# Optimization experiments

Measured on AMD Instinct MI355X. Metric: run time of the kernel, lower is better.

## Reference

```python
import jax, jax.numpy as jnp
import numpy as np


def setup_inputs() -> dict:
    key = jax.random.key(0)
    k1, k2, k3, k4 = jax.random.split(key, 4)
    B, N, F = 16, 2048, 512
    return {
        "source": jax.random.normal(k1, (B, N, 3), dtype=jnp.float32),
        "target": jax.random.normal(k2, (B, N, 3), dtype=jnp.float32),
        "fsource": jax.random.normal(k3, (B, F, N), dtype=jnp.float32),
        "ftarget": jax.random.normal(k4, (B, F, N), dtype=jnp.float32),
    }


def reference(source, target, fsource, ftarget):
    # source/target: (B, N, 3) -> (B, 3, N)
    src = jnp.swapaxes(source, 1, 2)
    tgt = jnp.swapaxes(target, 1, 2)

    # soft correspondence: logits[b, i, j] = <ftarget[b,:,i], fsource[b,:,j]>
    logits = jnp.einsum('bfi,bfj->bij', ftarget, fsource)  # (B, Nt, Ns)
    weight = jax.nn.softmax(logits, axis=1)  # softmax over target points (dim=1)

    # predicted target for each source point: (B, 3, Ns)
    pred_tgt = jnp.einsum('bci,bij->bcj', tgt, weight)

    src_mean = jnp.mean(src, axis=2, keepdims=True)        # (B, 3, 1)
    tgt_mean = jnp.mean(pred_tgt, axis=2, keepdims=True)   # (B, 3, 1)
    src_res = src - src_mean
    tgt_res = pred_tgt - tgt_mean

    # 3x3 cross-covariance per batch item
    S = jnp.einsum('bcn,bdn->bcd', src_res, tgt_res)  # (B, 3, 3)

    # torch.svd: S = U diag(Sig) V^T ; jnp.linalg.svd: S = U diag(Sig) Vh
    U, Sig, Vh = jnp.linalg.svd(S, full_matrices=False)
    V = jnp.swapaxes(Vh, 1, 2)
    UT = jnp.swapaxes(U, 1, 2)

    d = jnp.linalg.det(jnp.matmul(V, UT))  # (B,)
    B = S.shape[0]
    M = jnp.tile(jnp.eye(3, dtype=S.dtype)[None], (B, 1, 1))
    M = M.at[:, 2, 2].set(d)

    Rot = jnp.matmul(jnp.matmul(V, M), UT)                     # (B, 3, 3)
    tr = (tgt_mean - jnp.matmul(Rot, src_mean))[..., 0]        # (B, 3)
    return (Rot, tr)
```

## Files before the change

### kernel.cpp

```cpp
#include <hip/hip_runtime.h>
#include <math.h>
#include <stdint.h>

#define NB   16
#define NPT  2048
#define NF   512
#define BI   128
#define BJ   128
#define KB   32
#define NTHR 512
#define NJT  (NPT / BJ)
#define NIT  (NPT / BI)
#define NKC  (NF / KB)
#define NIQ  4

#define CGB1     1024
#define KCSLAB1  (128 * CGB1)
#define TPB1     ((size_t)NB * NKC * KCSLAB1)

#define CGS    1056
#define PLANE  8448
#define PLANE_H 4224
#define BPLANE 16896
#define BUF2   50688

typedef _Float16 h4 __attribute__((ext_vector_type(4)));
typedef _Float16 h8 __attribute__((ext_vector_type(8)));
typedef float    f32x4 __attribute__((ext_vector_type(4)));

#define TRR(dst, a) asm volatile("ds_read_b64_tr_b16 %0, %1" : "=v"(dst) : "v"(a))

#define MF(A, B, C) __builtin_amdgcn_mfma_f32_16x16x32_f16(A, B, C, 0, 0, 0)

__device__ __forceinline__ void gld16(const void* g, void* l) {
    __builtin_amdgcn_global_load_lds(
        (const __attribute__((address_space(1))) unsigned int*)g,
        (__attribute__((address_space(3))) unsigned int*)l, 16, 0, 0);
}

__device__ __forceinline__ h8 cat(h4 a, h4 b) {
    return __builtin_shufflevector(a, b, 0, 1, 2, 3, 4, 5, 6, 7);
}

__device__ __forceinline__ void cvt8(const float4 a, const float4 b, h8& hi, h8& lo) {
    hi[0] = (_Float16)a.x; hi[1] = (_Float16)a.y;
    hi[2] = (_Float16)a.z; hi[3] = (_Float16)a.w;
    hi[4] = (_Float16)b.x; hi[5] = (_Float16)b.y;
    hi[6] = (_Float16)b.z; hi[7] = (_Float16)b.w;
    lo[0] = (_Float16)(a.x - (float)hi[0]);
    lo[1] = (_Float16)(a.y - (float)hi[1]);
    lo[2] = (_Float16)(a.z - (float)hi[2]);
    lo[3] = (_Float16)(a.w - (float)hi[3]);
    lo[4] = (_Float16)(b.x - (float)hi[4]);
    lo[5] = (_Float16)(b.y - (float)hi[5]);
    lo[6] = (_Float16)(b.z - (float)hi[6]);
    lo[7] = (_Float16)(b.w - (float)hi[7]);
}

__device__ __forceinline__ h8 cvt8h(const float4 a, const float4 b) {
    h8 hi;
    hi[0] = (_Float16)a.x; hi[1] = (_Float16)a.y;
    hi[2] = (_Float16)a.z; hi[3] = (_Float16)a.w;
    hi[4] = (_Float16)b.x; hi[5] = (_Float16)b.y;
    hi[6] = (_Float16)b.z; hi[7] = (_Float16)b.w;
    return hi;
}

__device__ __forceinline__ int hoffB(int f, int n8) {
    return (n8 >> 1) * CGS + (f >> 4) * 512 + ((f >> 2) & 3) * 128
         + (f & 3) * 32 + (n8 & 1) * 16;
}

__global__ __launch_bounds__(256)
void prepass_kernel(const float* __restrict__ fsource,
                    const float* __restrict__ ftarget,
                    _Float16* __restrict__ tiled)
{
    const int b  = blockIdx.x;
    const int kc = blockIdx.y;
    const int z  = blockIdx.z;
    const int tensor = z >> 3;
    const int cgrp   = z & 7;
    const float* src = (tensor == 0 ? ftarget : fsource)
                     + (size_t)b * NF * NPT + (size_t)kc * KB * NPT + cgrp * 256;
    char* dst = (char*)tiled + (size_t)tensor * TPB1
              + ((size_t)(b * NKC + kc) * 128 + cgrp * 16) * CGB1;

    __shared__ _Float16 sm[8448];
    const int t   = threadIdx.x;
    const int kk8 = t >> 5;
    const int c8  = (t & 31) * 8;
    const int cg  = c8 >> 4;
    const int cl  = c8 & 15;

    #pragma unroll
    for (int rep = 0; rep < 4; ++rep) {
        const int k = rep * 8 + kk8;
        const float4 v0 = *(const float4*)(src + (size_t)k * NPT + c8);
        const float4 v1 = *(const float4*)(src + (size_t)k * NPT + c8 + 4);
        const h8 hi = cvt8h(v0, v1);
        const int kh = k >> 4, kr = k & 15, kg = kr >> 2, j = kr & 3;
        *(h8*)((char*)sm + cg * 1056 + kh * 512 + kg * 128 + j * 32 + cl * 2) = hi;
    }
    __syncthreads();
    #pragma unroll
    for (int q = 0; q < 4; ++q) {
        const int off = q * 4096 + t * 16;
        const int ocg = off >> 10, rem = off & 1023;
        *(float4*)(dst + off) = *(const float4*)((char*)sm + ocg * 1056 + rem);
    }
}

__global__ __launch_bounds__(256, 2)
void attn_state_tiled(const float* __restrict__ target,
                      const _Float16* __restrict__ tiled,
                      float* __restrict__ stw)
{
    const int b    = blockIdx.x;
    const int jt   = blockIdx.y;
    const int iq   = blockIdx.z;
    const int j0   = jt * BJ;
    const int tid  = threadIdx.x;
    const int lane = tid & 63;
    const int wave = tid >> 6;
    const int wi   = wave >> 1;
    const int wj   = wave & 1;
    const int lg   = lane >> 4;
    const int lr   = lane & 15;

    __shared__ __align__(16) char TIL[2][32768];
    __shared__ float  tgtsAll[3][512];
    __shared__ float  redM[2][BJ];
    __shared__ float4 redS[2][BJ];

    const uint32_t tilesBase = (uint32_t)(uintptr_t)&TIL[0][0];
    const uint32_t trLane    = (uint32_t)(lane * 8);

    const char* Atile = (const char*)tiled;
    const char* Btile = (const char*)tiled + TPB1;

    {
        const float* tg = target + ((size_t)b * NPT + iq * 512) * 3;
        #pragma unroll
        for (int k = 0; k < 6; ++k) {
            const int p = tid + k * 256;
            tgtsAll[p % 3][p / 3] = tg[p];
        }
    }
    __syncthreads();

    float Mrun[4], Zrun[4], Yrun[4][3];
    #pragma unroll
    for (int n = 0; n < 4; ++n) {
        Mrun[n] = -3.0e38f; Zrun[n] = 0.0f;
        Yrun[n][0] = 0.0f; Yrun[n][1] = 0.0f; Yrun[n][2] = 0.0f;
    }

#define STAGE2(kc2v, dstbuf) { \
    const size_t slab0 = (size_t)(b * NKC + 2 * (kc2v)) * KCSLAB1; \
    const size_t slab1 = slab0 + KCSLAB1; \
    const size_t aoff  = (size_t)(i0 >> 4) * CGB1 + lane * 16; \
    const size_t boff  = (size_t)(j0 >> 4) * CGB1 + lane * 16; \
    char* lb = &TIL[dstbuf][0]; \
    gld16(Atile + slab0 + aoff + wave * 1024,       lb + wave * 1024); \
    gld16(Atile + slab0 + aoff + (wave + 4) * 1024, lb + (wave + 4) * 1024); \
    gld16(Atile + slab1 + aoff + wave * 1024,       lb + 8192 + wave * 1024); \
    gld16(Atile + slab1 + aoff + (wave + 4) * 1024, lb + 8192 + (wave + 4) * 1024); \
    gld16(Btile + slab0 + boff + wave * 1024,       lb + 16384 + wave * 1024); \
    gld16(Btile + slab0 + boff + (wave + 4) * 1024, lb + 16384 + (wave + 4) * 1024); \
    gld16(Btile + slab1 + boff + wave * 1024,       lb + 24576 + wave * 1024); \
    gld16(Btile + slab1 + boff + (wave + 4) * 1024, lb + 24576 + (wave + 4) * 1024); }

#define RD_A1(m) TRR(ta[m][0], aB + (m) * CGB1); \
                 TRR(ta[m][1], aB + (m) * CGB1 + 512);
#define RD_B1(n) TRR(tb[n][0], bB + (n) * CGB1); \
                 TRR(tb[n][1], bB + (n) * CGB1 + 512);
#define WAITK(N) asm volatile("s_waitcnt lgkmcnt(" #N ")" ::: "memory"); \
                 __builtin_amdgcn_sched_barrier(0);
#define MROW1(M) \
    { const h8 Ah = cat(ta[M][0], ta[M][1]); \
      acc[M][0] = MF(Ah, Bh[0], acc[M][0]); \
      acc[M][1] = MF(Ah, Bh[1], acc[M][1]); \
      acc[M][2] = MF(Ah, Bh[2], acc[M][2]); \
      acc[M][3] = MF(Ah, Bh[3], acc[M][3]); }

#define KHALF(hofs) { \
    const uint32_t aB = bufB + (hofs) + (uint32_t)(wi * 4) * CGB1 + trLane; \
    const uint32_t bB = bufB + 16384u + (hofs) + (uint32_t)(wj * 4) * CGB1 + trLane; \
    h4 ta[4][2], tb[4][2]; \
    h8 Bh[4]; \
    RD_A1(0) RD_B1(0) RD_B1(1) RD_B1(2) RD_B1(3) \
    RD_A1(1) RD_A1(2) RD_A1(3) \
    WAITK(6) \
    Bh[0] = cat(tb[0][0], tb[0][1]); \
    Bh[1] = cat(tb[1][0], tb[1][1]); \
    Bh[2] = cat(tb[2][0], tb[2][1]); \
    Bh[3] = cat(tb[3][0], tb[3][1]); \
    MROW1(0) \
    WAITK(4) MROW1(1) \
    WAITK(2) MROW1(2) \
    WAITK(0) MROW1(3) }

    for (int it = 0; it < 4; ++it) {
        const int i0 = iq * 512 + it * BI;

        STAGE2(0, 0)
        asm volatile("s_waitcnt vmcnt(0)" ::: "memory");
        __builtin_amdgcn_sched_barrier(0);
        __syncthreads();

        f32x4 acc[4][4];
        #pragma unroll
        for (int m = 0; m < 4; ++m)
            #pragma unroll
            for (int n = 0; n < 4; ++n)
                acc[m][n] = (f32x4){0.0f, 0.0f, 0.0f, 0.0f};

        for (int kc2 = 0; kc2 < 8; ++kc2) {
            const int buf = kc2 & 1;
            if (kc2 + 1 < 8) STAGE2(kc2 + 1, buf ^ 1)

            const uint32_t bufB = tilesBase + (uint32_t)buf * 32768;
            __builtin_amdgcn_s_setprio(1);
            KHALF(0u)
            KHALF(8192u)
            __builtin_amdgcn_s_setprio(0);

            asm volatile("s_waitcnt vmcnt(0)" ::: "memory");
            __builtin_amdgcn_sched_barrier(0);
            __syncthreads();
        }

        #pragma unroll
        for (int n = 0; n < 4; ++n) {
            float m = acc[0][n][0];
            #pragma unroll
            for (int mm = 0; mm < 4; ++mm)
                #pragma unroll
                for (int r = 0; r < 4; ++r)
                    m = fmaxf(m, acc[mm][n][r]);
            m = fmaxf(m, __shfl_xor(m, 16));
            m = fmaxf(m, __shfl_xor(m, 32));
            if (lane < 16) redM[wi][wj * 64 + n * 16 + lr] = m;
        }
        __syncthreads();
        float mnew[4];
        #pragma unroll
        for (int n = 0; n < 4; ++n) {
            const int col = wj * 64 + n * 16 + lr;
            mnew[n] = fmaxf(Mrun[n], fmaxf(redM[0][col], redM[1][col]));
        }

        float z[4] = {0, 0, 0, 0}, y[4][3] = {{0,0,0},{0,0,0},{0,0,0},{0,0,0}};
        #pragma unroll
        for (int mm = 0; mm < 4; ++mm)
            #pragma unroll
            for (int r = 0; r < 4; ++r) {
                const int iL = it * BI + wi * 64 + mm * 16 + lg * 4 + r;
                const float t0 = tgtsAll[0][iL], t1 = tgtsAll[1][iL], t2 = tgtsAll[2][iL];
                #pragma unroll
                for (int n = 0; n < 4; ++n) {
                    const float e = __expf(acc[mm][n][r] - mnew[n]);
                    z[n] += e;
                    y[n][0] = fmaf(e, t0, y[n][0]);
                    y[n][1] = fmaf(e, t1, y[n][1]);
                    y[n][2] = fmaf(e, t2, y[n][2]);
                }
            }
        #pragma unroll
        for (int n = 0; n < 4; ++n) {
            #pragma unroll
            for (int off = 16; off <= 32; off <<= 1) {
                z[n]    += __shfl_xor(z[n], off);
                y[n][0] += __shfl_xor(y[n][0], off);
                y[n][1] += __shfl_xor(y[n][1], off);
                y[n][2] += __shfl_xor(y[n][2], off);
            }
            if (lane < 16)
                redS[wi][wj * 64 + n * 16 + lr] = make_float4(z[n], y[n][0], y[n][1], y[n][2]);
        }
        __syncthreads();
        #pragma unroll
        for (int n = 0; n < 4; ++n) {
            const int col = wj * 64 + n * 16 + lr;
            const float4 s0 = redS[0][col], s1 = redS[1][col];
            const float sc = __expf(Mrun[n] - mnew[n]);
            Zrun[n]    = Zrun[n]    * sc + s0.x + s1.x;
            Yrun[n][0] = Yrun[n][0] * sc + s0.y + s1.y;
            Yrun[n][1] = Yrun[n][1] * sc + s0.z + s1.z;
            Yrun[n][2] = Yrun[n][2] * sc + s0.w + s1.w;
            Mrun[n] = mnew[n];
        }
        __syncthreads();
    }

    if (wi == 0 && lane < 16) {
        const int SP4 = NB * NIQ * NPT;
        #pragma unroll
        for (int n = 0; n < 4; ++n) {
            const int j   = j0 + wj * 64 + n * 16 + lr;
            const int idx = (b * NIQ + iq) * NPT + j;
            stw[idx]           = Mrun[n];
            stw[SP4 + idx]     = Zrun[n];
            stw[2 * SP4 + idx] = Yrun[n][0];
            stw[3 * SP4 + idx] = Yrun[n][1];
            stw[4 * SP4 + idx] = Yrun[n][2];
        }
    }
#undef STAGE2
#undef RD_A1
#undef RD_B1
#undef WAITK
#undef MROW1
#undef KHALF
}

__global__ void combine4_kernel(const float* __restrict__ source,
                                const float* __restrict__ stw,
                                float* __restrict__ partials)
{
    const int b   = blockIdx.x;
    const int jc  = blockIdx.y;
    const int tid = threadIdx.x;
    const int lane = tid & 63, wv = tid >> 6;
    const int j = jc * BJ + tid;
    const int SP = NB * NIQ * NPT;

    __shared__ float fin2[2][15];

    float m[NIQ], zz[NIQ], yy0[NIQ], yy1[NIQ], yy2[NIQ];
    #pragma unroll
    for (int q = 0; q < NIQ; ++q) {
        const int idx = (b * NIQ + q) * NPT + j;
        m[q]   = stw[idx];
        zz[q]  = stw[SP + idx];
        yy0[q] = stw[2 * SP + idx];
        yy1[q] = stw[3 * SP + idx];
        yy2[q] = stw[4 * SP + idx];
    }
    float ms = m[0];
    #pragma unroll
    for (int q = 1; q < NIQ; ++q) ms = fmaxf(ms, m[q]);
    float Z = 0, Y0 = 0, Y1 = 0, Y2 = 0;
    #pragma unroll
    for (int q = 0; q < NIQ; ++q) {
        const float s = __expf(m[q] - ms);
        Z  += zz[q]  * s;
        Y0 += yy0[q] * s;
        Y1 += yy1[q] * s;
        Y2 += yy2[q] * s;
    }
    const float iz = 1.0f / Z;
    const float p0 = Y0 * iz, p1 = Y1 * iz, p2 = Y2 * iz;

    const float* sp = source + ((size_t)b * NPT + j) * 3;
    const float s0 = sp[0], s1 = sp[1], s2 = sp[2];

    float v[15];
    v[0] = s0; v[1] = s1; v[2] = s2;
    v[3] = p0; v[4] = p1; v[5] = p2;
    v[6]  = s0 * p0; v[7]  = s0 * p1; v[8]  = s0 * p2;
    v[9]  = s1 * p0; v[10] = s1 * p1; v[11] = s1 * p2;
    v[12] = s2 * p0; v[13] = s2 * p1; v[14] = s2 * p2;

    #pragma unroll
    for (int q = 0; q < 15; ++q)
        #pragma unroll
        for (int off = 32; off > 0; off >>= 1)
            v[q] += __shfl_down(v[q], off);
    if (lane == 0) {
        #pragma unroll
        for (int q = 0; q < 15; ++q) fin2[wv][q] = v[q];
    }
    __syncthreads();
    if (tid == 0) {
        float* o = partials + (((size_t)b << 4) + jc) * 16;
        #pragma unroll
        for (int q = 0; q < 15; ++q) o[q] = fin2[0][q] + fin2[1][q];
    }
}

__global__ void combine_kernel(const float* __restrict__ source,
                               const float* __restrict__ stw,
                               float* __restrict__ partials)
{
    const int b   = blockIdx.x;
    const int jc  = blockIdx.y;
    const int tid = threadIdx.x;
    const int lane = tid & 63, wv = tid >> 6;
    const int j = jc * BJ + tid;
    const int SP = NB * 2 * NPT;
    const int i0 = (b * 2 + 0) * NPT + j;
    const int i1 = (b * 2 + 1) * NPT + j;

    __shared__ float fin2[2][15];

    const float ma = stw[i0],      mb = stw[i1];
    const float za = stw[SP + i0], zb = stw[SP + i1];
    const float ms = fmaxf(ma, mb);
    const float sa = __expf(ma - ms), sb = __expf(mb - ms);
    const float zt = za * sa + zb * sb;
    const float iz = 1.0f / zt;
    const float p0 = (stw[2 * SP + i0] * sa + stw[2 * SP + i1] * sb) * iz;
    const float p1 = (stw[3 * SP + i0] * sa + stw[3 * SP + i1] * sb) * iz;
    const float p2 = (stw[4 * SP + i0] * sa + stw[4 * SP + i1] * sb) * iz;

    const float* sp = source + ((size_t)b * NPT + j) * 3;
    const float s0 = sp[0], s1 = sp[1], s2 = sp[2];

    float v[15];
    v[0] = s0; v[1] = s1; v[2] = s2;
    v[3] = p0; v[4] = p1; v[5] = p2;
    v[6]  = s0 * p0; v[7]  = s0 * p1; v[8]  = s0 * p2;
    v[9]  = s1 * p0; v[10] = s1 * p1; v[11] = s1 * p2;
    v[12] = s2 * p0; v[13] = s2 * p1; v[14] = s2 * p2;

    #pragma unroll
    for (int q = 0; q < 15; ++q)
        #pragma unroll
        for (int off = 32; off > 0; off >>= 1)
            v[q] += __shfl_down(v[q], off);
    if (lane == 0) {
        #pragma unroll
        for (int q = 0; q < 15; ++q) fin2[wv][q] = v[q];
    }
    __syncthreads();
    if (tid == 0) {
        float* o = partials + (((size_t)b << 4) + jc) * 16;
        #pragma unroll
        for (int q = 0; q < 15; ++q) o[q] = fin2[0][q] + fin2[1][q];
    }
}

__global__ __launch_bounds__(NTHR, 2)
void attn_state_kernel(const float* __restrict__ target,
                       const float* __restrict__ fsource,
                       const float* __restrict__ ftarget,
                       float* __restrict__ stw)
{
    const int b    = blockIdx.x;
    const int jt   = blockIdx.y;
    const int ih   = blockIdx.z;
    const int j0   = jt * 256;
    const int tid  = threadIdx.x;
    const int lane = tid & 63;
    const int wave = tid >> 6;
    const int wi   = wave >> 2;
    const int wj   = wave & 3;
    const int lg   = lane >> 4;
    const int lr   = lane & 15;

    __shared__ __align__(16) unsigned char TIL[2][BUF2];
    __shared__ float  tgts[3][BI];
    __shared__ float  redM[2][256];
    __shared__ float4 redS[2][256];

    const uint32_t tilesBase = (uint32_t)(uintptr_t)&TIL[0][0];
    const uint32_t trLane    = (uint32_t)(lane * 8);
    const size_t   fbase     = (size_t)b * NF * NPT;

    const int fA  = tid >> 4,  n8A  = tid & 15;
    const int fB0 = tid >> 5,  n8B  = tid & 31;
    const int fB1 = (tid + 512) >> 5;
    const int offA  = hoffB(fA, n8A);
    const int offB0 = hoffB(fB0, n8B);
    const int offB1 = hoffB(fB1, n8B);

    float Mrun[4], Zrun[4], Yrun[4][3];
    #pragma unroll
    for (int n = 0; n < 4; ++n) {
        Mrun[n] = -3.0e38f; Zrun[n] = 0.0f;
        Yrun[n][0] = 0.0f; Yrun[n][1] = 0.0f; Yrun[n][2] = 0.0f;
    }

#define RD_B(n) TRR(tb[n][0][0], bB + (n) * CGS); \
                TRR(tb[n][0][1], bB + (n) * CGS + 512); \
                TRR(tb[n][1][0], bB + (n) * CGS + BPLANE); \
                TRR(tb[n][1][1], bB + (n) * CGS + BPLANE + 512);
#define RD_A(m) TRR(ta[m][0][0], aB + (m) * CGS); \
                TRR(ta[m][0][1], aB + (m) * CGS + 512); \
                TRR(ta[m][1][0], aB + (m) * CGS + PLANE); \
                TRR(ta[m][1][1], aB + (m) * CGS + PLANE + 512);
#define BBLD(n) Bh[n] = cat(tb[n][0][0], tb[n][0][1]); \
                Bl[n] = cat(tb[n][1][0], tb[n][1][1]);
#define MM3(M, N) \
    acc[M][N] = MF(Ah, Bh[N], acc[M][N]); \
    acc[M][N] = MF(Ah, Bl[N], acc[M][N]); \
    acc[M][N] = MF(Al, Bh[N], acc[M][N]);
#define MSTEP(M, WAITSTR) \
    asm volatile("s_waitcnt lgkmcnt(" WAITSTR ")" ::: "memory"); \
    __builtin_amdgcn_sched_barrier(0); \
    { const h8 Ah = cat(ta[M][0][0], ta[M][0][1]); \
      const h8 Al = cat(ta[M][1][0], ta[M][1][1]); \
      MM3(M, 0) MM3(M, 1) MM3(M, 2) MM3(M, 3) }

    for (int it = 0; it < 8; ++it) {
        const int i0 = ih * 1024 + it * BI;

        const float* pA  = ftarget + fbase + (size_t)fA  * NPT + i0 + n8A * 8;
        const float* pB0 = fsource + fbase + (size_t)fB0 * NPT + j0 + n8B * 8;
        const float* pB1 = fsource + fbase + (size_t)fB1 * NPT + j0 + n8B * 8;

        {
            float4 a0  = *(const float4*)(pA);
            float4 a1  = *(const float4*)(pA + 4);
            float4 b00 = *(const float4*)(pB0);
            float4 b01 = *(const float4*)(pB0 + 4);
            float4 b10 = *(const float4*)(pB1);
            float4 b11 = *(const float4*)(pB1 + 4);
            if (tid < BI) {
                const float* tp = target + ((size_t)b * NPT + i0 + tid) * 3;
                tgts[0][tid] = tp[0]; tgts[1][tid] = tp[1]; tgts[2][tid] = tp[2];
            }
            unsigned char* bp = (unsigned char*)&TIL[0][0];
            h8 hi, lo;
            cvt8(a0, a1, hi, lo);
            *(h8*)(bp + offA) = hi;  *(h8*)(bp + PLANE + offA) = lo;
            cvt8(b00, b01, hi, lo);
            *(h8*)(bp + 2 * PLANE + offB0) = hi;  *(h8*)(bp + 2 * PLANE + BPLANE + offB0) = lo;
            cvt8(b10, b11, hi, lo);
            *(h8*)(bp + 2 * PLANE + offB1) = hi;  *(h8*)(bp + 2 * PLANE + BPLANE + offB1) = lo;
        }
        __syncthreads();

        f32x4 acc[4][4];
        #pragma unroll
        for (int m = 0; m < 4; ++m)
            #pragma unroll
            for (int n = 0; n < 4; ++n)
                acc[m][n] = (f32x4){0.0f, 0.0f, 0.0f, 0.0f};

        for (int kc = 0; kc < NKC; ++kc) {
            const int buf = kc & 1;
            float4 ga0, ga1, gb00, gb01, gb10, gb11;
            if (kc + 1 < NKC) {
                const size_t ko = (size_t)(kc + 1) * KB * NPT;
                ga0  = *(const float4*)(pA + ko);
                ga1  = *(const float4*)(pA + ko + 4);
                gb00 = *(const float4*)(pB0 + ko);
                gb01 = *(const float4*)(pB0 + ko + 4);
                gb10 = *(const float4*)(pB1 + ko);
                gb11 = *(const float4*)(pB1 + ko + 4);
            }

            const uint32_t bb = tilesBase + (uint32_t)buf * BUF2;
            const uint32_t aB = bb + (uint32_t)(wi * 4) * CGS + trLane;
            const uint32_t bB = bb + 2u * PLANE + (uint32_t)(wj * 4) * CGS + trLane;
            h4 ta[4][2][2], tb[4][2][2];
            h8 Bh[4], Bl[4];

            __builtin_amdgcn_s_setprio(1);
            RD_B(0) RD_B(1) RD_B(2) RD_B(3)
            RD_A(0) RD_A(1) RD_A(2) RD_A(3)
            asm volatile("s_waitcnt lgkmcnt(12)" ::: "memory");
            __builtin_amdgcn_sched_barrier(0);
            BBLD(0) BBLD(1) BBLD(2) BBLD(3)
            {
                const h8 Ah = cat(ta[0][0][0], ta[0][0][1]);
                const h8 Al = cat(ta[0][1][0], ta[0][1][1]);
                MM3(0, 0) MM3(0, 1) MM3(0, 2) MM3(0, 3)
            }
            MSTEP(1, "8")
            MSTEP(2, "4")
            MSTEP(3, "0")
            __builtin_amdgcn_s_setprio(0);

            if (kc + 1 < NKC) {
                unsigned char* bp = (unsigned char*)&TIL[0][0] + (buf ^ 1) * BUF2;
                h8 hi, lo;
                cvt8(ga0, ga1, hi, lo);
                *(h8*)(bp + offA) = hi;  *(h8*)(bp + PLANE + offA) = lo;
                cvt8(gb00, gb01, hi, lo);
                *(h8*)(bp + 2 * PLANE + offB0) = hi;  *(h8*)(bp + 2 * PLANE + BPLANE + offB0) = lo;
                cvt8(gb10, gb11, hi, lo);
                *(h8*)(bp + 2 * PLANE + offB1) = hi;  *(h8*)(bp + 2 * PLANE + BPLANE + offB1) = lo;
                __syncthreads();
            }
        }

        #pragma unroll
        for (int n = 0; n < 4; ++n) {
            float m = acc[0][n][0];
            #pragma unroll
            for (int mm = 0; mm < 4; ++mm)
                #pragma unroll
                for (int r = 0; r < 4; ++r)
                    m = fmaxf(m, acc[mm][n][r]);
            m = fmaxf(m, __shfl_xor(m, 16));
            m = fmaxf(m, __shfl_xor(m, 32));
            if (lane < 16) redM[wi][wj * 64 + n * 16 + lr] = m;
        }
        __syncthreads();
        float mnew[4];
        #pragma unroll
        for (int n = 0; n < 4; ++n) {
            const int col = wj * 64 + n * 16 + lr;
            mnew[n] = fmaxf(Mrun[n], fmaxf(redM[0][col], redM[1][col]));
        }

        float z[4] = {0, 0, 0, 0}, y[4][3] = {{0,0,0},{0,0,0},{0,0,0},{0,0,0}};
        #pragma unroll
        for (int mm = 0; mm < 4; ++mm)
            #pragma unroll
            for (int r = 0; r < 4; ++r) {
                const int iL = wi * 64 + mm * 16 + lg * 4 + r;
                const float t0 = tgts[0][iL], t1 = tgts[1][iL], t2 = tgts[2][iL];
                #pragma unroll
                for (int n = 0; n < 4; ++n) {
                    const float e = __expf(acc[mm][n][r] - mnew[n]);
                    z[n] += e;
                    y[n][0] = fmaf(e, t0, y[n][0]);
                    y[n][1] = fmaf(e, t1, y[n][1]);
                    y[n][2] = fmaf(e, t2, y[n][2]);
                }
            }
        #pragma unroll
        for (int n = 0; n < 4; ++n) {
            #pragma unroll
            for (int off = 16; off <= 32; off <<= 1) {
                z[n]    += __shfl_xor(z[n], off);
                y[n][0] += __shfl_xor(y[n][0], off);
                y[n][1] += __shfl_xor(y[n][1], off);
                y[n][2] += __shfl_xor(y[n][2], off);
            }
            if (lane < 16)
                redS[wi][wj * 64 + n * 16 + lr] = make_float4(z[n], y[n][0], y[n][1], y[n][2]);
        }
        __syncthreads();
        #pragma unroll
        for (int n = 0; n < 4; ++n) {
            const int col = wj * 64 + n * 16 + lr;
            const float4 s0 = redS[0][col], s1 = redS[1][col];
            const float sc = __expf(Mrun[n] - mnew[n]);
            Zrun[n]    = Zrun[n]    * sc + s0.x + s1.x;
            Yrun[n][0] = Yrun[n][0] * sc + s0.y + s1.y;
            Yrun[n][1] = Yrun[n][1] * sc + s0.z + s1.z;
            Yrun[n][2] = Yrun[n][2] * sc + s0.w + s1.w;
            Mrun[n] = mnew[n];
        }
        __syncthreads();
    }

    if (wi == 0 && lane < 16) {
        #pragma unroll
        for (int n = 0; n < 4; ++n) {
            const int j   = j0 + wj * 64 + n * 16 + lr;
            const int idx = (b * 2 + ih) * NPT + j;
            stw[0 * (NB * 2 * NPT) + idx] = Mrun[n];
            stw[1 * (NB * 2 * NPT) + idx] = Zrun[n];
            stw[2 * (NB * 2 * NPT) + idx] = Yrun[n][0];
            stw[3 * (NB * 2 * NPT) + idx] = Yrun[n][1];
            stw[4 * (NB * 2 * NPT) + idx] = Yrun[n][2];
        }
    }
#undef RD_B
#undef RD_A
#undef BBLD
#undef MM3
#undef MSTEP
}

__device__ inline void jrot(float A[3][3], float V[3][3], int p, int q)
{
    const float apq = A[p][q];
    if (fabsf(apq) < 1e-28f) return;
    const float tau = (A[q][q] - A[p][p]) / (2.0f * apq);
    const float t   = (tau >= 0.0f ? 1.0f : -1.0f) / (fabsf(tau) + sqrtf(1.0f + tau * tau));
    const float c   = rsqrtf(1.0f + t * t);
    const float s   = t * c;
    const float app = A[p][p], aqq = A[q][q];
    A[p][p] = app - t * apq;
    A[q][q] = aqq + t * apq;
    A[p][q] = 0.0f; A[q][p] = 0.0f;
    const int r = 3 - p - q;
    const float arp = A[r][p], arq = A[r][q];
    A[r][p] = c * arp - s * arq; A[p][r] = A[r][p];
    A[r][q] = s * arp + c * arq; A[q][r] = A[r][q];
    #pragma unroll
    for (int rr = 0; rr < 3; ++rr) {
        const float vrp = V[rr][p], vrq = V[rr][q];
        V[rr][p] = c * vrp - s * vrq;
        V[rr][q] = s * vrp + c * vrq;
    }
}

__global__ void svd_finalize_kernel(const float* __restrict__ partials,
                                    float* __restrict__ out)
{
    const int b = threadIdx.x;
    if (b >= NB) return;

    float srcS[3] = {0, 0, 0}, predS[3] = {0, 0, 0}, SP[9] = {0, 0, 0, 0, 0, 0, 0, 0, 0};
    for (int p = 0; p < NJT; ++p) {
        const float* vv = partials + (((size_t)b << 4) + p) * 16;
        srcS[0] += vv[0]; srcS[1] += vv[1]; srcS[2] += vv[2];
        predS[0] += vv[3]; predS[1] += vv[4]; predS[2] += vv[5];
        #pragma unroll
        for (int q = 0; q < 9; ++q) SP[q] += vv[6 + q];
    }

    const float invN = 1.0f / (float)NPT;
    float ms[3], mt[3];
    #pragma unroll
    for (int c = 0; c < 3; ++c) { ms[c] = srcS[c] * invN; mt[c] = predS[c] * invN; }

    float S[3][3];
    #pragma unroll
    for (int c = 0; c < 3; ++c)
        #pragma unroll
        for (int d = 0; d < 3; ++d)
            S[c][d] = SP[c * 3 + d] - srcS[c] * predS[d] * invN;

    float A[3][3];
    #pragma unroll
    for (int i = 0; i < 3; ++i)
        #pragma unroll
        for (int j = 0; j < 3; ++j)
            A[i][j] = S[0][i] * S[0][j] + S[1][i] * S[1][j] + S[2][i] * S[2][j];

    float V[3][3] = {{1, 0, 0}, {0, 1, 0}, {0, 0, 1}};
    for (int sweep = 0; sweep < 12; ++sweep) {
        jrot(A, V, 0, 1);
        jrot(A, V, 0, 2);
        jrot(A, V, 1, 2);
    }

    float lam[3] = {A[0][0], A[1][1], A[2][2]};
    for (int i = 0; i < 2; ++i) {
        int mx = i;
        for (int j = i + 1; j < 3; ++j) if (lam[j] > lam[mx]) mx = j;
        if (mx != i) {
            const float tl = lam[i]; lam[i] = lam[mx]; lam[mx] = tl;
            #pragma unroll
            for (int r = 0; r < 3; ++r) {
                const float tv = V[r][i]; V[r][i] = V[r][mx]; V[r][mx] = tv;
            }
        }
    }

    float w0[3], w1[3], u1[3], u2[3], u3[3];
    #pragma unroll
    for (int r = 0; r < 3; ++r) {
        w0[r] = S[r][0] * V[0][0] + S[r][1] * V[1][0] + S[r][2] * V[2][0];
        w1[r] = S[r][0] * V[0][1] + S[r][1] * V[1][1] + S[r][2] * V[2][1];
    }
    const float n1 = sqrtf(w0[0] * w0[0] + w0[1] * w0[1] + w0[2] * w0[2]) + 1e-30f;
    #pragma unroll
    for (int r = 0; r < 3; ++r) u1[r] = w0[r] / n1;
    const float d01 = u1[0] * w1[0] + u1[1] * w1[1] + u1[2] * w1[2];
    #pragma unroll
    for (int r = 0; r < 3; ++r) u2[r] = w1[r] - d01 * u1[r];
    const float n2 = sqrtf(u2[0] * u2[0] + u2[1] * u2[1] + u2[2] * u2[2]) + 1e-30f;
    #pragma unroll
    for (int r = 0; r < 3; ++r) u2[r] /= n2;
    u3[0] = u1[1] * u2[2] - u1[2] * u2[1];
    u3[1] = u1[2] * u2[0] - u1[0] * u2[2];
    u3[2] = u1[0] * u2[1] - u1[1] * u2[0];

    const float detV =
        V[0][0] * (V[1][1] * V[2][2] - V[1][2] * V[2][1]) -
        V[0][1] * (V[1][0] * V[2][2] - V[1][2] * V[2][0]) +
        V[0][2] * (V[1][0] * V[2][1] - V[1][1] * V[2][0]);

    float R[3][3];
    #pragma unroll
    for (int r = 0; r < 3; ++r)
        #pragma unroll
        for (int c = 0; c < 3; ++c)
            R[r][c] = V[r][0] * u1[c] + V[r][1] * u2[c] + detV * V[r][2] * u3[c];

    #pragma unroll
    for (int r = 0; r < 3; ++r)
        #pragma unroll
        for (int c = 0; c < 3; ++c)
            out[b * 9 + r * 3 + c] = R[r][c];

    #pragma unroll
    for (int r = 0; r < 3; ++r) {
        const float tr = mt[r] - (R[r][0] * ms[0] + R[r][1] * ms[1] + R[r][2] * ms[2]);
        out[NB * 9 + b * 3 + r] = tr;
    }
}

extern "C" void kernel_launch(void* const* d_in, const int* in_sizes, int n_in,
                              void* d_out, int out_size, void* d_ws, size_t ws_size,
                              hipStream_t stream)
{
    const float* source  = (const float*)d_in[0];
    const float* target  = (const float*)d_in[1];
    const float* fsource = (const float*)d_in[2];
    const float* ftarget = (const float*)d_in[3];
    float* out = (float*)d_out;

    const size_t PART_FLOATS = (size_t)NB * 16 * 16;
    const size_t ST4_FLOATS  = (size_t)5 * NB * NIQ * NPT;
    const size_t ST2_FLOATS  = (size_t)5 * NB * 2 * NPT;
    const size_t NEED_BIG    = 2 * TPB1 + (ST4_FLOATS + PART_FLOATS) * 4;

    if (ws_size >= NEED_BIG) {
        _Float16* tiled = (_Float16*)d_ws;
        float* stw      = (float*)((char*)d_ws + 2 * TPB1);
        float* partials = stw + ST4_FLOATS;
        prepass_kernel<<<dim3(NB, NKC, 16), 256, 0, stream>>>(fsource, ftarget, tiled);
        attn_state_tiled<<<dim3(NB, 16, NIQ), 256, 0, stream>>>(target, tiled, stw);
        combine4_kernel<<<dim3(NB, 16), 128, 0, stream>>>(source, stw, partials);
        svd_finalize_kernel<<<1, 64, 0, stream>>>(partials, out);
    } else {
        float* stw      = (float*)d_ws;
        float* partials = stw + ST2_FLOATS;
        attn_state_kernel<<<dim3(NB, 8, 2), NTHR, 0, stream>>>(target, fsource, ftarget, stw);
        combine_kernel<<<dim3(NB, 16), 128, 0, stream>>>(source, stw, partials);
        svd_finalize_kernel<<<1, 64, 0, stream>>>(partials, out);
    }
}
```

Measured before the change: 144.8 us.

## Give each wave a private LDS staging buffer and drop block-wide barriers in k-loop

Each wave now loads only the A and B sub-tiles it consumes into its own LDS region (wave-private double buffer, 16 KB per wave). The per-k-chunk __syncthreads is removed, leaving only a vmcnt wait. The goal is to stop waves stalling on each other in the main GEMM loop. In exchange, the k-loop now runs 16 single-chunk steps instead of 8 double-chunk steps. A tiles are re-fetched by the two waves sharing wi and B tiles by the two sharing wj, which doubles global/L2 traffic per block.

```diff
diff --git a/kernel.cpp b/kernel.cpp
--- a/kernel.cpp
+++ b/kernel.cpp
@@ -128,16 +128,19 @@
     const int lg   = lane >> 4;
     const int lr   = lane & 15;
 
-    __shared__ __align__(16) char TIL[2][32768];
+    __shared__ __align__(16) char TIL[4][16384];
     __shared__ float  tgtsAll[3][512];
     __shared__ float  redM[2][BJ];
     __shared__ float4 redS[2][BJ];
 
-    const uint32_t tilesBase = (uint32_t)(uintptr_t)&TIL[0][0];
-    const uint32_t trLane    = (uint32_t)(lane * 8);
+    const uint32_t trLane = (uint32_t)(lane * 8);
+    char* const TILW = &TIL[wave][0];
+    const uint32_t wBase = (uint32_t)(uintptr_t)TILW;
 
     const char* Atile = (const char*)tiled;
     const char* Btile = (const char*)tiled + TPB1;
+    const size_t slab0 = (size_t)(b * NKC) * KCSLAB1 + lane * 16;
+    const size_t thrB  = slab0 + (size_t)((j0 >> 4) + wj * 4) * CGB1;
 
     {
         const float* tg = target + ((size_t)b * NPT + iq * 512) * 3;
@@ -156,26 +159,26 @@
         Yrun[n][0] = 0.0f; Yrun[n][1] = 0.0f; Yrun[n][2] = 0.0f;
     }
 
-#define STAGE2(kc2v, dstbuf) { \
-    const size_t slab0 = (size_t)(b * NKC + 2 * (kc2v)) * KCSLAB1; \
-    const size_t slab1 = slab0 + KCSLAB1; \
-    const size_t aoff  = (size_t)(i0 >> 4) * CGB1 + lane * 16; \
-    const size_t boff  = (size_t)(j0 >> 4) * CGB1 + lane * 16; \
-    char* lb = &TIL[dstbuf][0]; \
-    gld16(Atile + slab0 + aoff + wave * 1024,       lb + wave * 1024); \
-    gld16(Atile + slab0 + aoff + (wave + 4) * 1024, lb + (wave + 4) * 1024); \
-    gld16(Atile + slab1 + aoff + wave * 1024,       lb + 8192 + wave * 1024); \
-    gld16(Atile + slab1 + aoff + (wave + 4) * 1024, lb + 8192 + (wave + 4) * 1024); \
-    gld16(Btile + slab0 + boff + wave * 1024,       lb + 16384 + wave * 1024); \
-    gld16(Btile + slab0 + boff + (wave + 4) * 1024, lb + 16384 + (wave + 4) * 1024); \
-    gld16(Btile + slab1 + boff + wave * 1024,       lb + 24576 + wave * 1024); \
-    gld16(Btile + slab1 + boff + (wave + 4) * 1024, lb + 24576 + (wave + 4) * 1024); }
-
-#define RD_A1(m) TRR(ta[m][0], aB + (m) * CGB1); \
-                 TRR(ta[m][1], aB + (m) * CGB1 + 512);
-#define RD_B1(n) TRR(tb[n][0], bB + (n) * CGB1); \
-                 TRR(tb[n][1], bB + (n) * CGB1 + 512);
+#define STAGEW(kcv, bufv) { \
+    const char* pa = Atile + thrA + (size_t)(kcv) * KCSLAB1; \
+    const char* pb = Btile + thrB + (size_t)(kcv) * KCSLAB1; \
+    char* lb = TILW + (bufv) * 8192; \
+    gld16(pa,        lb); \
+    gld16(pa + 1024, lb + 1024); \
+    gld16(pa + 2048, lb + 2048); \
+    gld16(pa + 3072, lb + 3072); \
+    gld16(pb,        lb + 4096); \
+    gld16(pb + 1024, lb + 5120); \
+    gld16(pb + 2048, lb + 6144); \
+    gld16(pb + 3072, lb + 7168); }
+
+#define RD_A1(m) TRR(ta[m][0], aB + (m) * 1024); \
+                 TRR(ta[m][1], aB + (m) * 1024 + 512);
+#define RD_B1(n) TRR(tb[n][0], bB + (n) * 1024); \
+                 TRR(tb[n][1], bB + (n) * 1024 + 512);
 #define WAITK(N) asm volatile("s_waitcnt lgkmcnt(" #N ")" ::: "memory"); \
+                 __builtin_amdgcn_sched_barrier(0);
+#define WAITV0   asm volatile("s_waitcnt vmcnt(0)" ::: "memory"); \
                  __builtin_amdgcn_sched_barrier(0);
 #define MROW1(M) \
     { const h8 Ah = cat(ta[M][0], ta[M][1]); \
@@ -184,9 +187,9 @@
       acc[M][2] = MF(Ah, Bh[2], acc[M][2]); \
       acc[M][3] = MF(Ah, Bh[3], acc[M][3]); }
 
-#define KHALF(hofs) { \
-    const uint32_t aB = bufB + (hofs) + (uint32_t)(wi * 4) * CGB1 + trLane; \
-    const uint32_t bB = bufB + 16384u + (hofs) + (uint32_t)(wj * 4) * CGB1 + trLane; \
+#define KSTEPW(bufv) { \
+    const uint32_t aB = wBase + (bufv) * 8192u + trLane; \
+    const uint32_t bB = aB + 4096u; \
     h4 ta[4][2], tb[4][2]; \
     h8 Bh[4]; \
     RD_A1(0) RD_B1(0) RD_B1(1) RD_B1(2) RD_B1(3) \
@@ -203,11 +206,10 @@
 
     for (int it = 0; it < 4; ++it) {
         const int i0 = iq * 512 + it * BI;
-
-        STAGE2(0, 0)
-        asm volatile("s_waitcnt vmcnt(0)" ::: "memory");
-        __builtin_amdgcn_sched_barrier(0);
-        __syncthreads();
+        const size_t thrA = slab0 + (size_t)((i0 >> 4) + wi * 4) * CGB1;
+
+        STAGEW(0, 0)
+        WAITV0
 
         f32x4 acc[4][4];
         #pragma unroll
@@ -216,19 +218,15 @@
             for (int n = 0; n < 4; ++n)
                 acc[m][n] = (f32x4){0.0f, 0.0f, 0.0f, 0.0f};
 
-        for (int kc2 = 0; kc2 < 8; ++kc2) {
-            const int buf = kc2 & 1;
-            if (kc2 + 1 < 8) STAGE2(kc2 + 1, buf ^ 1)
-
-            const uint32_t bufB = tilesBase + (uint32_t)buf * 32768;
+        for (int kc = 0; kc < NKC; ++kc) {
+            const int buf = kc & 1;
+            if (kc + 1 < NKC) STAGEW(kc + 1, buf ^ 1)
+
             __builtin_amdgcn_s_setprio(1);
-            KHALF(0u)
-            KHALF(8192u)
+            KSTEPW(buf)
             __builtin_amdgcn_s_setprio(0);
 
-            asm volatile("s_waitcnt vmcnt(0)" ::: "memory");
-            __builtin_amdgcn_sched_barrier(0);
-            __syncthreads();
+            WAITV0
         }
 
         #pragma unroll
@@ -307,12 +305,13 @@
             stw[4 * SP4 + idx] = Yrun[n][2];
         }
     }
-#undef STAGE2
+#undef STAGEW
 #undef RD_A1
 #undef RD_B1
 #undef WAITK
+#undef WAITV0
 #undef MROW1
-#undef KHALF
+#undef KSTEPW
 }
 
 __global__ void combine4_kernel(const float* __restrict__ source,
```

After: 153.1 us. +5.8%, slower.
